# Optimization experiments

Hardware: AMD Instinct MI355X
Metric: run time of the kernel (lower is better)

The kernel has to match this reference:

```python
import jax, jax.numpy as jnp
import numpy as np
import math

B, S, D = 4, 2048, 1024
NUM_HEADS = 16
HEAD_DIM = D // NUM_HEADS


def setup_inputs() -> dict:
    key = jax.random.key(0)
    ks = jax.random.split(key, 6)
    scale = 1.0 / math.sqrt(D)
    batch = jax.random.normal(ks[0], (B, S, D), dtype=jnp.float32)
    w_query = jax.random.normal(ks[1], (D, D), dtype=jnp.float32) * scale
    w_key = jax.random.normal(ks[2], (D, D), dtype=jnp.float32) * scale
    w_value = jax.random.normal(ks[3], (D, D), dtype=jnp.float32) * scale
    out_w = jax.random.normal(ks[4], (D, D), dtype=jnp.float32) * scale
    out_b = jax.random.normal(ks[5], (D,), dtype=jnp.float32) * 0.01
    return {"batch": batch, "w_query": w_query, "w_key": w_key,
            "w_value": w_value, "out_w": out_w, "out_b": out_b}


def reference(batch, w_query, w_key, w_value, out_w, out_b):
    b, s, _ = batch.shape
    # QKV projections (Linear with no bias): x @ W^T, here weights stored as [D,D] applied as x@W
    q = (batch @ w_query).reshape(b, s, NUM_HEADS, HEAD_DIM)
    k = (batch @ w_key).reshape(b, s, NUM_HEADS, HEAD_DIM)
    v = (batch @ w_value).reshape(b, s, NUM_HEADS, HEAD_DIM)
    # scores: [b, h, s, s]
    scores = jnp.einsum('bqhd,bkhd->bhqk', q, k)
    causal = jnp.tril(jnp.ones((s, s), dtype=bool))
    scores = jnp.where(causal, scores, -jnp.inf)
    # original divides by sqrt(head_dim) AFTER masking (-inf stays -inf)
    weights = jax.nn.softmax(scores / math.sqrt(HEAD_DIM), axis=-1)
    # dropout_percent = 0 -> identity
    out = jnp.einsum('bhqk,bkhd->bqhd', weights, v).reshape(b, s, D)
    return out @ out_w + out_b
```

## Files before the change

### kernel.cpp

```cpp
#include <hip/hip_runtime.h>
#include <hip/hip_bf16.h>

#define S_LEN 2048
#define D_DIM 1024
#define NHEAD 16
#define HDIM  64
#define BATCH 4
#define MROWS (BATCH*S_LEN)

typedef short bf16x8 __attribute__((ext_vector_type(8)));
typedef float f32x4  __attribute__((ext_vector_type(4)));
typedef float f32x16 __attribute__((ext_vector_type(16)));
typedef unsigned short u16;

#if __has_builtin(__builtin_amdgcn_exp2f)
#define EXP2(x) __builtin_amdgcn_exp2f(x)
#else
#define EXP2(x) __expf((x) * 0.6931471805599453f)
#endif

#define BAR() asm volatile("s_barrier" ::: "memory")
#define WAITV0() asm volatile("s_waitcnt vmcnt(0)" ::: "memory")

__device__ inline u16 f2bf(float f) {
  union { float f; unsigned u; } v; v.f = f;
  unsigned r = v.u + 0x7fff + ((v.u >> 16) & 1);
  return (u16)(r >> 16);
}

__device__ inline unsigned cvtpk(float lo, float hi_) {
  unsigned d;
  asm("v_cvt_pk_bf16_f32 %0, %1, %2" : "=v"(d) : "v"(lo), "v"(hi_));
  return d;
}

__device__ inline void perm32swap(unsigned& a, unsigned& b) {
  asm volatile("v_permlane32_swap_b32 %0, %1" : "+v"(a), "+v"(b));
}

__device__ inline void gload_lds16(const void* g, void* l) {
  __builtin_amdgcn_global_load_lds(
      (const __attribute__((address_space(1))) void*)g,
      (__attribute__((address_space(3))) void*)l, 16, 0, 0);
}

__global__ void cvt_x_kernel(const float* __restrict__ x, u16* __restrict__ xb, int n4) {
  int i = blockIdx.x * 256 + threadIdx.x;
  if (i >= n4) return;
  float4 v = reinterpret_cast<const float4*>(x)[i];
  ushort4 o;
  o.x = f2bf(v.x); o.y = f2bf(v.y); o.z = f2bf(v.z); o.w = f2bf(v.w);
  reinterpret_cast<ushort4*>(xb)[i] = o;
}

__global__ void transpose_w4_kernel(const float* __restrict__ wq, const float* __restrict__ wk,
                                    const float* __restrict__ wv, const float* __restrict__ wo,
                                    u16* __restrict__ wqkvT, u16* __restrict__ woT) {
  __shared__ float t[32][33];
  int z = blockIdx.z;
  const float* w = (z == 0) ? wq : (z == 1) ? wk : (z == 2) ? wv : wo;
  u16* wt = (z < 3) ? (wqkvT + (size_t)z * 1024 * 1024) : woT;
  int tx = threadIdx.x, ty = threadIdx.y;
  int n0 = blockIdx.x * 32, k0 = blockIdx.y * 32;
#pragma unroll
  for (int j = 0; j < 32; j += 8)
    t[ty + j][tx] = w[(size_t)(k0 + ty + j) * D_DIM + n0 + tx];
  __syncthreads();
#pragma unroll
  for (int j = 0; j < 32; j += 8)
    wt[(size_t)(n0 + ty + j) * D_DIM + k0 + tx] = f2bf(t[tx][ty + j]);
}

template <int EPI>
__global__ __launch_bounds__(256) void gemm_bt_kernel(
    const u16* __restrict__ A, const u16* __restrict__ Bt,
    void* __restrict__ Cv, u16* __restrict__ KP, u16* __restrict__ VP,
    const float* __restrict__ bias) {
  __shared__ u16 lA[2][128 * 32];
  __shared__ u16 lB[2][128 * 32];
  const int tid = threadIdx.x, wid = tid >> 6, lane = tid & 63;
  const int bm = blockIdx.y, bn = blockIdx.x;
  const int fr = lane & 15, fq = lane >> 4;
  const int r0 = wid * 32;
  const int srow = lane >> 2, scol = (lane & 3) * 8;
  const u16* gA = A + (size_t)(bm * 128 + r0 + srow) * 1024 + scol;
  const u16* gB = Bt + (size_t)(bn * 128 + r0 + srow) * 1024 + scol;

  f32x4 acc[4][4] = {};
  const int wm = (wid >> 1) * 64, wn = (wid & 1) * 64;

  gload_lds16(gA,             &lA[0][r0 * 32]);
  gload_lds16(gA + 16 * 1024, &lA[0][r0 * 32 + 16 * 32]);
  gload_lds16(gB,             &lB[0][r0 * 32]);
  gload_lds16(gB + 16 * 1024, &lB[0][r0 * 32 + 16 * 32]);
  WAITV0();
  BAR();

#pragma unroll
  for (int k0 = 0; k0 < 1024; k0 += 32) {
    const int cur = (k0 >> 5) & 1, nxt = cur ^ 1;
    if (k0 + 32 < 1024) {
      gload_lds16(gA + k0 + 32,             &lA[nxt][r0 * 32]);
      gload_lds16(gA + k0 + 32 + 16 * 1024, &lA[nxt][r0 * 32 + 16 * 32]);
      gload_lds16(gB + k0 + 32,             &lB[nxt][r0 * 32]);
      gload_lds16(gB + k0 + 32 + 16 * 1024, &lB[nxt][r0 * 32 + 16 * 32]);
    }
    bf16x8 fa[4], fb[4];
#pragma unroll
    for (int i = 0; i < 4; i++) {
      fa[i] = *(const bf16x8*)&lA[cur][(wm + i * 16 + fr) * 32 + fq * 8];
      fb[i] = *(const bf16x8*)&lB[cur][(wn + i * 16 + fr) * 32 + fq * 8];
    }
#pragma unroll
    for (int i = 0; i < 4; i++)
#pragma unroll
      for (int j = 0; j < 4; j++)
        acc[i][j] = __builtin_amdgcn_mfma_f32_16x16x32_bf16(fa[i], fb[j], acc[i][j], 0, 0, 0);
    WAITV0();
    BAR();
  }

  if (EPI == 1) {
#pragma unroll
    for (int i = 0; i < 4; i++)
#pragma unroll
      for (int j = 0; j < 4; j++)
#pragma unroll
        for (int r = 0; r < 4; r++) {
          int row = bm * 128 + wm + i * 16 + fq * 4 + r;
          int col = bn * 128 + wn + j * 16 + fr;
          ((float*)Cv)[(size_t)row * 1024 + col] = acc[i][j][r] + bias[col];
        }
    return;
  }

  const int col0 = bn * 128;
  if (col0 < 1024) {
#pragma unroll
    for (int i = 0; i < 4; i++)
#pragma unroll
      for (int j = 0; j < 4; j++)
#pragma unroll
        for (int r = 0; r < 4; r++) {
          int row = bm * 128 + wm + i * 16 + fq * 4 + r;
          int col = col0 + wn + j * 16 + fr;
          ((u16*)Cv)[(size_t)row * 1024 + col] = f2bf(acc[i][j][r]);
        }
  } else if (col0 < 2048) {
#pragma unroll
    for (int i = 0; i < 4; i++)
#pragma unroll
      for (int j = 0; j < 4; j++) {
        int col = col0 + wn + j * 16 + fr;
        int ck = col - 1024;
        int h = ck >> 6, d = ck & 63;
        int sfr = d >> 4, e = d & 7, hb = (d >> 3) & 1;
#pragma unroll
        for (int r = 0; r < 4; r++) {
          int row = bm * 128 + wm + i * 16 + fq * 4 + r;
          int b = row >> 11, sp = row & 2047;
          int bh = b * 16 + h, jt = sp >> 5;
          int lanep = (sp & 31) + 32 * hb;
          KP[((size_t)(bh * 64 + jt) * 4 + sfr) * 512 + lanep * 8 + e] = f2bf(acc[i][j][r]);
        }
      }
  } else {
#pragma unroll
    for (int i = 0; i < 4; i++)
#pragma unroll
      for (int j = 0; j < 4; j++) {
        int col = col0 + wn + j * 16 + fr;
        int cv = col - 2048;
        int h = cv >> 6, d = cv & 63;
        int R0 = bm * 128 + wm + i * 16 + fq * 4;
        int b = R0 >> 11, sp0 = R0 & 2047;
        int bh = b * 16 + h, jt = sp0 >> 5;
        int c = (d >> 5) * 2 + ((sp0 >> 4) & 1);
        int lanep = (d & 31) + 32 * ((sp0 >> 3) & 1);
        int e0 = sp0 & 7;
        ushort4 ov;
        ov.x = f2bf(acc[i][j][0]); ov.y = f2bf(acc[i][j][1]);
        ov.z = f2bf(acc[i][j][2]); ov.w = f2bf(acc[i][j][3]);
        *(ushort4*)(VP + ((size_t)(bh * 64 + jt) * 4 + c) * 512 + lanep * 8 + e0) = ov;
      }
  }
}

__global__ __launch_bounds__(256) void attn_kernel(
    const u16* __restrict__ Q, const u16* __restrict__ KP,
    const u16* __restrict__ VP, u16* __restrict__ O) {
  const int tid = threadIdx.x, wid = tid >> 6, lane = tid & 63;
  const int lq = lane & 31, hi = lane >> 5;
  int f = blockIdx.x;
  int xcd = f & 7, kk = f >> 3;
  int bh = xcd * 8 + (kk & 7);
  int qblk = 15 - (kk >> 3);
  int b = bh >> 4, h = bh & 15;
  int q0 = qblk * 128 + wid * 32;
  int q = q0 + lq;

  const u16* Qrow = Q + (size_t)(b * S_LEN + q) * D_DIM + h * HDIM;
  bf16x8 qf[4];
#pragma unroll
  for (int s = 0; s < 4; s++)
    qf[s] = *(const bf16x8*)(Qrow + s * 16 + hi * 8);

  const bf16x8* KPt = (const bf16x8*)KP + (size_t)bh * 64 * 4 * 64;
  const bf16x8* VPt = (const bf16x8*)VP + (size_t)bh * 64 * 4 * 64;

  f32x16 acc0 = {}, acc1 = {};
  float m = -3.0e38f, l = 0.f;
  const int nt = qblk * 4 + wid + 1;

  for (int t = 0; t < nt; ++t) {
    const int j0 = t * 32;
    const size_t fb = (size_t)t * 4 * 64 + lane;
    bf16x8 kf0 = KPt[fb], kf1 = KPt[fb + 64], kf2 = KPt[fb + 128], kf3 = KPt[fb + 192];
    bf16x8 vf00 = VPt[fb], vf01 = VPt[fb + 64], vf10 = VPt[fb + 128], vf11 = VPt[fb + 192];

    f32x16 sa = {};
    __builtin_amdgcn_s_setprio(1);
    sa = __builtin_amdgcn_mfma_f32_32x32x16_bf16(kf0, qf[0], sa, 0, 0, 0);
    sa = __builtin_amdgcn_mfma_f32_32x32x16_bf16(kf1, qf[1], sa, 0, 0, 0);
    sa = __builtin_amdgcn_mfma_f32_32x32x16_bf16(kf2, qf[2], sa, 0, 0, 0);
    sa = __builtin_amdgcn_mfma_f32_32x32x16_bf16(kf3, qf[3], sa, 0, 0, 0);
    __builtin_amdgcn_s_setprio(0);

    float p[16];
#pragma unroll
    for (int r = 0; r < 16; ++r) p[r] = sa[r] * 0.1803368801f;

    if (t == nt - 1) {
#pragma unroll
      for (int r = 0; r < 16; ++r) {
        int kidx = j0 + (r & 3) + 8 * (r >> 2) + 4 * hi;
        if (kidx > q) p[r] = -3.0e38f;
      }
    }

    float x8[8], x4[4], x2[2];
#pragma unroll
    for (int i = 0; i < 8; ++i) x8[i] = fmaxf(p[2 * i], p[2 * i + 1]);
#pragma unroll
    for (int i = 0; i < 4; ++i) x4[i] = fmaxf(x8[2 * i], x8[2 * i + 1]);
    x2[0] = fmaxf(x4[0], x4[1]); x2[1] = fmaxf(x4[2], x4[3]);
    float pm = fmaxf(x2[0], x2[1]);
    pm = fmaxf(pm, __shfl_xor(pm, 32));

    if (__any(pm > m + 11.5f)) {
      float mn = fmaxf(m, pm);
      float sc = EXP2(m - mn);
      l *= sc;
#pragma unroll
      for (int r = 0; r < 16; ++r) { acc0[r] *= sc; acc1[r] *= sc; }
      m = mn;
    }

    float rs = 0.f;
#pragma unroll
    for (int r = 0; r < 16; ++r) { p[r] = EXP2(p[r] - m); rs += p[r]; }
    rs += __shfl_xor(rs, 32);
    l += rs;

    unsigned c0 = cvtpk(p[0],  p[1]),  c1 = cvtpk(p[2],  p[3]);
    unsigned c2 = cvtpk(p[4],  p[5]),  c3 = cvtpk(p[6],  p[7]);
    unsigned c4 = cvtpk(p[8],  p[9]),  c5 = cvtpk(p[10], p[11]);
    unsigned c6 = cvtpk(p[12], p[13]), c7 = cvtpk(p[14], p[15]);
    perm32swap(c0, c2); perm32swap(c1, c3);
    perm32swap(c4, c6); perm32swap(c5, c7);
    union U4 { unsigned u[4]; bf16x8 v; } F0, F1;
    F0.u[0] = c0; F0.u[1] = c1; F0.u[2] = c2; F0.u[3] = c3;
    F1.u[0] = c4; F1.u[1] = c5; F1.u[2] = c6; F1.u[3] = c7;

    __builtin_amdgcn_s_setprio(1);
    acc0 = __builtin_amdgcn_mfma_f32_32x32x16_bf16(vf00, F0.v, acc0, 0, 0, 0);
    acc0 = __builtin_amdgcn_mfma_f32_32x32x16_bf16(vf01, F1.v, acc0, 0, 0, 0);
    acc1 = __builtin_amdgcn_mfma_f32_32x32x16_bf16(vf10, F0.v, acc1, 0, 0, 0);
    acc1 = __builtin_amdgcn_mfma_f32_32x32x16_bf16(vf11, F1.v, acc1, 0, 0, 0);
    __builtin_amdgcn_s_setprio(0);
  }

  float inv = 1.f / l;
  u16* Orow = O + (size_t)(b * S_LEN + q) * D_DIM + h * HDIM;
#pragma unroll
  for (int g = 0; g < 4; ++g) {
    ushort4 o4;
    o4.x = f2bf(acc0[g * 4 + 0] * inv);
    o4.y = f2bf(acc0[g * 4 + 1] * inv);
    o4.z = f2bf(acc0[g * 4 + 2] * inv);
    o4.w = f2bf(acc0[g * 4 + 3] * inv);
    *(ushort4*)(Orow + 8 * g + 4 * hi) = o4;
  }
#pragma unroll
  for (int g = 0; g < 4; ++g) {
    ushort4 o4;
    o4.x = f2bf(acc1[g * 4 + 0] * inv);
    o4.y = f2bf(acc1[g * 4 + 1] * inv);
    o4.z = f2bf(acc1[g * 4 + 2] * inv);
    o4.w = f2bf(acc1[g * 4 + 3] * inv);
    *(ushort4*)(Orow + 32 + 8 * g + 4 * hi) = o4;
  }
}

extern "C" void kernel_launch(void* const* d_in, const int* in_sizes, int n_in,
                              void* d_out, int out_size, void* d_ws, size_t ws_size,
                              hipStream_t stream) {
  const float* x  = (const float*)d_in[0];
  const float* wq = (const float*)d_in[1];
  const float* wk = (const float*)d_in[2];
  const float* wv = (const float*)d_in[3];
  const float* wo = (const float*)d_in[4];
  const float* ob = (const float*)d_in[5];
  float* out = (float*)d_out;

  char* ws = (char*)d_ws;
  u16* Xb    = (u16*)(ws);
  u16* Ab    = (u16*)(ws);
  u16* Qb    = (u16*)(ws + (size_t)16 * 1024 * 1024);
  u16* KPb   = (u16*)(ws + (size_t)32 * 1024 * 1024);
  u16* VPb   = (u16*)(ws + (size_t)48 * 1024 * 1024);
  u16* WqkvT = (u16*)(ws + (size_t)64 * 1024 * 1024);
  u16* WoT   = (u16*)(ws + (size_t)70 * 1024 * 1024);

  cvt_x_kernel<<<(MROWS * D_DIM / 4) / 256, 256, 0, stream>>>(x, Xb, MROWS * D_DIM / 4);

  transpose_w4_kernel<<<dim3(32, 32, 4), dim3(32, 8), 0, stream>>>(
      wq, wk, wv, wo, WqkvT, WoT);

  gemm_bt_kernel<0><<<dim3(24, 64), 256, 0, stream>>>(
      Xb, WqkvT, Qb, KPb, VPb, nullptr);

  attn_kernel<<<dim3(1024), 256, 0, stream>>>(Qb, KPb, VPb, Ab);

  gemm_bt_kernel<1><<<dim3(8, 64), 256, 0, stream>>>(
      Ab, WoT, out, nullptr, nullptr, ob);
}
```

Baseline: 172.8 us.

## Fold softmax scale into Q projection and single-buffer QKV GEMM loop

Multiplies the softmax scale (log2e/sqrt(head_dim)) into Q in the QKV GEMM epilogue, which removes 16 per-element multiplies per tile in the attention inner loop. The QKV GEMM (EPI==0) also switches from a double-buffered LDS pipeline to a single-buffered load/sync/compute/sync loop. That halves its LDS footprint, possibly for occupancy, but it serializes the global loads with the MFMA work. Rounding Q to bf16 after scaling slightly changes numerics.

```diff
diff --git a/kernel.cpp b/kernel.cpp
--- a/kernel.cpp
+++ b/kernel.cpp
@@ -21,6 +21,7 @@
 
 #define BAR() asm volatile("s_barrier" ::: "memory")
 #define WAITV0() asm volatile("s_waitcnt vmcnt(0)" ::: "memory")
+#define QSCALE 0.1803368801111137f
 
 __device__ inline u16 f2bf(float f) {
   union { float f; unsigned u; } v; v.f = f;
@@ -76,8 +77,8 @@
     const u16* __restrict__ A, const u16* __restrict__ Bt,
     void* __restrict__ Cv, u16* __restrict__ KP, u16* __restrict__ VP,
     const float* __restrict__ bias) {
-  __shared__ u16 lA[2][128 * 32];
-  __shared__ u16 lB[2][128 * 32];
+  __shared__ u16 lA[EPI == 0 ? 1 : 2][128 * 32];
+  __shared__ u16 lB[EPI == 0 ? 1 : 2][128 * 32];
   const int tid = threadIdx.x, wid = tid >> 6, lane = tid & 63;
   const int bm = blockIdx.y, bn = blockIdx.x;
   const int fr = lane & 15, fq = lane >> 4;
@@ -89,35 +90,56 @@
   f32x4 acc[4][4] = {};
   const int wm = (wid >> 1) * 64, wn = (wid & 1) * 64;
 
-  gload_lds16(gA,             &lA[0][r0 * 32]);
-  gload_lds16(gA + 16 * 1024, &lA[0][r0 * 32 + 16 * 32]);
-  gload_lds16(gB,             &lB[0][r0 * 32]);
-  gload_lds16(gB + 16 * 1024, &lB[0][r0 * 32 + 16 * 32]);
-  WAITV0();
-  BAR();
-
-#pragma unroll
-  for (int k0 = 0; k0 < 1024; k0 += 32) {
-    const int cur = (k0 >> 5) & 1, nxt = cur ^ 1;
-    if (k0 + 32 < 1024) {
-      gload_lds16(gA + k0 + 32,             &lA[nxt][r0 * 32]);
-      gload_lds16(gA + k0 + 32 + 16 * 1024, &lA[nxt][r0 * 32 + 16 * 32]);
-      gload_lds16(gB + k0 + 32,             &lB[nxt][r0 * 32]);
-      gload_lds16(gB + k0 + 32 + 16 * 1024, &lB[nxt][r0 * 32 + 16 * 32]);
+  if (EPI == 0) {
+    for (int k0 = 0; k0 < 1024; k0 += 32) {
+      gload_lds16(gA + k0,             &lA[0][r0 * 32]);
+      gload_lds16(gA + k0 + 16 * 1024, &lA[0][r0 * 32 + 16 * 32]);
+      gload_lds16(gB + k0,             &lB[0][r0 * 32]);
+      gload_lds16(gB + k0 + 16 * 1024, &lB[0][r0 * 32 + 16 * 32]);
+      __syncthreads();
+      bf16x8 fa[4], fb[4];
+#pragma unroll
+      for (int i = 0; i < 4; i++) {
+        fa[i] = *(const bf16x8*)&lA[0][(wm + i * 16 + fr) * 32 + fq * 8];
+        fb[i] = *(const bf16x8*)&lB[0][(wn + i * 16 + fr) * 32 + fq * 8];
+      }
+#pragma unroll
+      for (int i = 0; i < 4; i++)
+#pragma unroll
+        for (int j = 0; j < 4; j++)
+          acc[i][j] = __builtin_amdgcn_mfma_f32_16x16x32_bf16(fa[i], fb[j], acc[i][j], 0, 0, 0);
+      __syncthreads();
     }
-    bf16x8 fa[4], fb[4];
-#pragma unroll
-    for (int i = 0; i < 4; i++) {
-      fa[i] = *(const bf16x8*)&lA[cur][(wm + i * 16 + fr) * 32 + fq * 8];
-      fb[i] = *(const bf16x8*)&lB[cur][(wn + i * 16 + fr) * 32 + fq * 8];
-    }
-#pragma unroll
-    for (int i = 0; i < 4; i++)
-#pragma unroll
-      for (int j = 0; j < 4; j++)
-        acc[i][j] = __builtin_amdgcn_mfma_f32_16x16x32_bf16(fa[i], fb[j], acc[i][j], 0, 0, 0);
+  } else {
+    gload_lds16(gA,             &lA[0][r0 * 32]);
+    gload_lds16(gA + 16 * 1024, &lA[0][r0 * 32 + 16 * 32]);
+    gload_lds16(gB,             &lB[0][r0 * 32]);
+    gload_lds16(gB + 16 * 1024, &lB[0][r0 * 32 + 16 * 32]);
     WAITV0();
     BAR();
+#pragma unroll
+    for (int k0 = 0; k0 < 1024; k0 += 32) {
+      const int cur = (k0 >> 5) & 1, nxt = cur ^ 1;
+      if (k0 + 32 < 1024) {
+        gload_lds16(gA + k0 + 32,             &lA[nxt][r0 * 32]);
+        gload_lds16(gA + k0 + 32 + 16 * 1024, &lA[nxt][r0 * 32 + 16 * 32]);
+        gload_lds16(gB + k0 + 32,             &lB[nxt][r0 * 32]);
+        gload_lds16(gB + k0 + 32 + 16 * 1024, &lB[nxt][r0 * 32 + 16 * 32]);
+      }
+      bf16x8 fa[4], fb[4];
+#pragma unroll
+      for (int i = 0; i < 4; i++) {
+        fa[i] = *(const bf16x8*)&lA[cur][(wm + i * 16 + fr) * 32 + fq * 8];
+        fb[i] = *(const bf16x8*)&lB[cur][(wn + i * 16 + fr) * 32 + fq * 8];
+      }
+#pragma unroll
+      for (int i = 0; i < 4; i++)
+#pragma unroll
+        for (int j = 0; j < 4; j++)
+          acc[i][j] = __builtin_amdgcn_mfma_f32_16x16x32_bf16(fa[i], fb[j], acc[i][j], 0, 0, 0);
+      WAITV0();
+      BAR();
+    }
   }
 
   if (EPI == 1) {
@@ -144,7 +166,7 @@
         for (int r = 0; r < 4; r++) {
           int row = bm * 128 + wm + i * 16 + fq * 4 + r;
           int col = col0 + wn + j * 16 + fr;
-          ((u16*)Cv)[(size_t)row * 1024 + col] = f2bf(acc[i][j][r]);
+          ((u16*)Cv)[(size_t)row * 1024 + col] = f2bf(acc[i][j][r] * QSCALE);
         }
   } else if (col0 < 2048) {
 #pragma unroll
@@ -228,7 +250,7 @@
 
     float p[16];
 #pragma unroll
-    for (int r = 0; r < 16; ++r) p[r] = sa[r] * 0.1803368801f;
+    for (int r = 0; r < 16; ++r) p[r] = sa[r];
 
     if (t == nt - 1) {
 #pragma unroll
```

Result: slower. 218.6 us (+26.5%).
